# Kernel tuning notes

Measured on AMD Instinct MI355X. Metric: run time of the kernel, lower is better.

Reference implementation:

```python
import jax, jax.numpy as jnp
import numpy as np

SIGMA_D = 0.2
SIGMA_A = 15.0
FACTOR_A = 180.0 / (SIGMA_A * np.pi)
HIDDEN = 256


def sinusoidal_embedding(x, d_model):
    # GeoTransformer-style: interleaved sin/cos pairs along last dim.
    div_term = jnp.exp(jnp.arange(0, d_model, 2, dtype=x.dtype) * (-np.log(10000.0) / d_model))  # (d/2,)
    omegas = x[..., None] * div_term  # (..., d/2)
    emb = jnp.stack([jnp.sin(omegas), jnp.cos(omegas)], axis=-1)  # (..., d/2, 2)
    return emb.reshape(*x.shape, d_model)


def _indices(points, anchor_points):
    # pairwise sq dist: |p|^2 + |a|^2 - 2 p.a, clamped at 0
    sq = (jnp.sum(points ** 2, -1)[:, :, None]
          + jnp.sum(anchor_points ** 2, -1)[:, None, :]
          - 2.0 * jnp.einsum('bnd,bkd->bnk', points, anchor_points))
    dist_map = jnp.sqrt(jnp.maximum(sq, 0.0))  # (B,N,K)
    d_indices = dist_map / SIGMA_D
    ref_vectors = points[:, :, None, :] - anchor_points[:, None, :, :]  # (B,N,K,3)
    # gather with indices [1,2,...,K-1,0] == roll by -1 along K
    anc_vectors = jnp.roll(ref_vectors, shift=-1, axis=2)
    sin_values = jnp.linalg.norm(jnp.cross(ref_vectors, anc_vectors, axis=-1), axis=-1)
    cos_values = jnp.sum(ref_vectors * anc_vectors, axis=-1)
    angles = jnp.arctan2(sin_values, cos_values)
    a_indices = angles * FACTOR_A
    return d_indices, a_indices


def setup_inputs() -> dict:
    key = jax.random.key(0)
    ks = jax.random.split(key, 5)
    B, N, K, H = 1, 4096, 64, HIDDEN
    return {
        'points': jax.random.normal(ks[0], (B, N, 3), jnp.float32),
        'anchor_points': jax.random.normal(ks[1], (B, K, 3), jnp.float32),
        'cor_score': jax.random.uniform(ks[2], (K,), jnp.float32),
        'Wa': jax.random.normal(ks[3], (H, H), jnp.float32) * (1.0 / np.sqrt(H)),
        'ba': jnp.zeros((H,), jnp.float32),
        'Wd': jax.random.normal(ks[4], (H, H), jnp.float32) * (1.0 / np.sqrt(H)),
        'bd': jnp.zeros((H,), jnp.float32),
    }


def reference(points, anchor_points, cor_score, Wa, ba, Wd, bd):
    d_idx, a_idx = _indices(points, anchor_points)  # computed under no_grad in torch
    d_idx = jax.lax.stop_gradient(d_idx)
    a_idx = jax.lax.stop_gradient(a_idx)
    a_emb = sinusoidal_embedding(a_idx, HIDDEN)          # (B,N,K,H)
    a_emb = jnp.einsum('bnkh,oh->bnko', a_emb, Wa) + ba
    d_emb = sinusoidal_embedding(d_idx, HIDDEN)
    d_emb = jnp.einsum('bnkh,oh->bnko', d_emb, Wd) + bd
    # reduction_a == 'max'
    d_emb = jnp.max(d_emb, axis=2)
    a_emb = jnp.max(a_emb, axis=2)
    return d_emb + a_emb  # (B,N,H)
```

## Files before the change

kernel.cpp:

```cpp
#include <hip/hip_runtime.h>
#include <hip/hip_bf16.h>
#include <math.h>


typedef __attribute__((ext_vector_type(8))) short short8;
typedef __attribute__((ext_vector_type(16))) float f32x16;
typedef __attribute__((ext_vector_type(4))) unsigned int uint4v;

#define HH 256
#define KK 112
#define P_PTS 8
#define NPTS 4096

__device__ __forceinline__ unsigned short f2bf(float f) {
    union { float f; unsigned int u; } v; v.f = f;
    unsigned int r = v.u + 0x7fffu + ((v.u >> 16) & 1u);
    return (unsigned short)(r >> 16);
}

__device__ __forceinline__ unsigned int pack_sc(float s, float c) {
    union { __hip_bfloat162 h; unsigned int u; } v;
    v.h = __float22bfloat162_rn(make_float2(s, c));
    return v.u;
}

__global__ __launch_bounds__(256)
void prep_w_kernel(const float* __restrict__ Wa, const float* __restrict__ Wd,
                   unsigned short* __restrict__ wbf) {
    const int t = blockIdx.x;
    const int o = threadIdx.x;
    const float* W = (t == 0 ? Wd : Wa) + o * HH;
    unsigned short* dst = wbf + (t * HH + o) * KK;
    for (int e = 0; e < 104; ++e) dst[e] = f2bf(W[e]);
    float u1 = 0.f, u2 = 0.f, u3 = 0.f, u4 = 0.f, v = 0.f;
    for (int i = 52; i < 128; ++i) {
        const float d = exp2f(-(float)i * 0.10381025296523008f);
        const float d2 = d * d;
        const float ws = W[2 * i], wc = W[2 * i + 1];
        u1 += d * ws;
        u3 += -(d * d2) * (1.0f / 6.0f) * ws;
        u2 += -0.5f * d2 * wc;
        u4 += (d2 * d2) * (1.0f / 24.0f) * wc;
        v  += wc;
    }
    dst[104] = f2bf(u1);
    dst[105] = f2bf(u2);
    dst[106] = f2bf(u3);
    dst[107] = f2bf(u4);
    dst[108] = f2bf(v);
    dst[109] = 0; dst[110] = 0; dst[111] = 0;
}


__global__ __launch_bounds__(512, 4)
void cgse_main(const float* __restrict__ points,
               const float* __restrict__ anchors,
               const unsigned short* __restrict__ wbf,
               const float* __restrict__ ba,
               const float* __restrict__ bd,
               float* __restrict__ out) {
    __shared__ __align__(16) unsigned short E[2][64 * 128];
    __shared__ float dms[2][P_PTS][HH];
    __shared__ float ams[2][P_PTS][HH];
    __shared__ float xs[2][P_PTS][64];
    __shared__ float anch[192];

    const int tid = threadIdx.x;
    const int wave = tid >> 6, lane = tid & 63;
    const int l5 = lane & 31, half = lane >> 5;
    const int base = blockIdx.x * P_PTS;
    const int hh = wave >> 2;
    const int colb = (wave & 3) * 64;

    if (tid < 192) anch[tid] = anchors[tid];
    __syncthreads();
    {
        const int k2 = (lane + 1) & 63;
        const int pn = base + wave;
        const float px = points[pn * 3 + 0], py = points[pn * 3 + 1], pz = points[pn * 3 + 2];
        const float r1x = px - anch[lane * 3 + 0];
        const float r1y = py - anch[lane * 3 + 1];
        const float r1z = pz - anch[lane * 3 + 2];
        const float r2x = px - anch[k2 * 3 + 0];
        const float r2y = py - anch[k2 * 3 + 1];
        const float r2z = pz - anch[k2 * 3 + 2];
        xs[0][wave][lane] = sqrtf(r1x * r1x + r1y * r1y + r1z * r1z) * 5.0f;
        const float cx = r1y * r2z - r1z * r2y;
        const float cy = r1z * r2x - r1x * r2z;
        const float cz = r1x * r2y - r1y * r2x;
        const float sv = sqrtf(cx * cx + cy * cy + cz * cz);
        const float cv = r1x * r2x + r1y * r2y + r1z * r2z;
        xs[1][wave][lane] = atan2f(sv, cv) * 3.8197186342054885f;
    }

    const float bias_c = (tid < HH) ? (ba[tid] + bd[tid]) : 0.0f;

    const float cw = 0.15915494309189535f * __expf(-(float)wave * 0.2878231366242554f);

    const int wbase = (lane << 8) ^ (((lane & 7) ^ wave) << 4);
    const int arow = hh * 32 + l5;
    const int rbase = (arow << 8) ^ ((arow & 7) << 4) ^ (half << 4);

    auto fill_chunk = [&](char* eb, int c, float x, float xc) {
        uint4v w;
        if (wave == 5 && c == 1) {
            const float x2 = x * x;
            w[0] = pack_sc(x, x2);
            w[1] = pack_sc(x2 * x, x2 * x2);
            w[2] = pack_sc(1.0f, 0.0f);
            w[3] = 0u;
        } else {
            const float t0 = c ? xc * 0.1f : xc;
            const float t[4] = {t0, t0 * 0.9305720409297085f,
                                t0 * 0.8659643233600653f, t0 * 0.8058421877614819f};
            #pragma unroll
            for (int j = 0; j < 4; ++j)
                w[j] = pack_sc(__builtin_amdgcn_sinf(t[j]), __builtin_amdgcn_cosf(t[j]));
        }
        *(uint4v*)(eb + (wbase ^ (c << 7))) = w;
    };

    short8 bw[2][7];
    auto loadW = [&](int t) {
        #pragma unroll
        for (int ntp = 0; ntp < 2; ++ntp) {
            const unsigned short* wr =
                wbf + (t * HH + colb + ntp * 32 + l5) * KK + half * 8;
            #pragma unroll
            for (int ks = 0; ks < 7; ++ks)
                bw[ntp][ks] = *(const short8*)(wr + ks * 16);
        }
    };

    loadW(0);
    __syncthreads();
    {
        const float x = xs[0][0][lane], xc = x * cw;
        fill_chunk((char*)E[0], 0, x, xc);
        if (wave < 6) fill_chunk((char*)E[0], 1, x, xc);
    }

    #pragma unroll 1
    for (int ph = 0; ph < 17; ++ph) {
        __syncthreads();

        if (ph >= 9 && tid < HH) {
            const int q = ph - 9;
            out[(base + q) * HH + tid] =
                fmaxf(ams[0][q][tid], ams[1][q][tid]) +
                fmaxf(dms[0][q][tid], dms[1][q][tid]) + bias_c;
        }
        if (ph == 16) break;

        const int b = ph & 1;
        if (ph == 8) loadW(1);

        const bool dofill = (ph + 1) < 16;
        float xn = 0.f, xcn = 0.f;
        if (dofill) {
            const int pn = (ph + 1) & 7;
            xn = ((ph + 1) < 8 ? xs[0][pn][lane] : xs[1][pn][lane]);
            xcn = xn * cw;
        }

        const char* ebC = (const char*)E[b];
        char* ebN = (char*)E[b ^ 1];

        f32x16 acc[2];
        #pragma unroll
        for (int ntp = 0; ntp < 2; ++ntp)
            #pragma unroll
            for (int r = 0; r < 16; ++r) acc[ntp][r] = 0.f;

        #pragma unroll
        for (int ks = 0; ks < 7; ++ks) {
            if (dofill) {
                if (ks == 0) fill_chunk(ebN, 0, xn, xcn);
                if (ks == 3 && wave < 6) fill_chunk(ebN, 1, xn, xcn);
            }
            const short8 afr = *(const short8*)(ebC + (rbase ^ (ks << 5)));
            acc[0] = __builtin_amdgcn_mfma_f32_32x32x16_bf16(afr, bw[0][ks], acc[0], 0, 0, 0);
            acc[1] = __builtin_amdgcn_mfma_f32_32x32x16_bf16(afr, bw[1][ks], acc[1], 0, 0, 0);
        }

        const int q = ph & 7;
        float (*pm)[P_PTS][HH] = (ph < 8) ? dms : ams;
        #pragma unroll
        for (int ntp = 0; ntp < 2; ++ntp) {
            float t8[8];
            #pragma unroll
            for (int r = 0; r < 8; ++r)
                t8[r] = fmaxf(acc[ntp][2 * r], acc[ntp][2 * r + 1]);
            const float ta = fmaxf(fmaxf(t8[0], t8[1]), fmaxf(t8[2], t8[3]));
            const float tb = fmaxf(fmaxf(t8[4], t8[5]), fmaxf(t8[6], t8[7]));
            float m = fmaxf(ta, tb);
            m = fmaxf(m, __shfl_down(m, 32));
            if (lane < 32) pm[hh][q][colb + ntp * 32 + l5] = m;
        }
    }
}

extern "C" void kernel_launch(void* const* d_in, const int* in_sizes, int n_in,
                              void* d_out, int out_size, void* d_ws, size_t ws_size,
                              hipStream_t stream) {
    const float* points  = (const float*)d_in[0];
    const float* anchors = (const float*)d_in[1];
    const float* Wa = (const float*)d_in[3];
    const float* ba = (const float*)d_in[4];
    const float* Wd = (const float*)d_in[5];
    const float* bd = (const float*)d_in[6];

    unsigned short* wbf = (unsigned short*)d_ws;

    hipLaunchKernelGGL(prep_w_kernel, dim3(2), dim3(256), 0, stream, Wa, Wd, wbf);
    hipLaunchKernelGGL(cgse_main, dim3(NPTS / P_PTS), dim3(512), 0, stream,
                       points, anchors, wbf, ba, bd, (float*)d_out);
}
```

Baseline: 110.5 us.

## Halve points per block, raise occupancy, vectorize weight prep, prioritize MFMA

The main kernel now handles 4 points per block instead of 8, which doubles the grid, and its launch bounds now ask for 6 blocks per CU. The weight prep kernel spreads its work over 8 blocks of 64 threads, loads and converts weights in float4 vectors, and replaces the per-iteration exp2 with a running multiply. It also raises wave priority around the MFMA pair and regroups the max reduction into 3-input fmax ops. Each block still loads both weight sets, so fewer points per block means more weight reloads per point, and the tighter register budget may cause spills.

```diff
diff --git a/kernel.cpp b/kernel.cpp
--- a/kernel.cpp
+++ b/kernel.cpp
@@ -6,10 +6,12 @@
 typedef __attribute__((ext_vector_type(8))) short short8;
 typedef __attribute__((ext_vector_type(16))) float f32x16;
 typedef __attribute__((ext_vector_type(4))) unsigned int uint4v;
+typedef __attribute__((ext_vector_type(4))) float float4v;
+typedef __attribute__((ext_vector_type(4))) unsigned short ushort4v;
 
 #define HH 256
 #define KK 112
-#define P_PTS 8
+#define P_PTS 4
 #define NPTS 4096
 
 __device__ __forceinline__ unsigned short f2bf(float f) {
@@ -24,17 +26,24 @@
     return v.u;
 }
 
-__global__ __launch_bounds__(256)
+__global__ __launch_bounds__(64)
 void prep_w_kernel(const float* __restrict__ Wa, const float* __restrict__ Wd,
                    unsigned short* __restrict__ wbf) {
-    const int t = blockIdx.x;
-    const int o = threadIdx.x;
+    const int r = blockIdx.x * 64 + threadIdx.x;
+    const int t = r >> 8, o = r & 255;
     const float* W = (t == 0 ? Wd : Wa) + o * HH;
     unsigned short* dst = wbf + (t * HH + o) * KK;
-    for (int e = 0; e < 104; ++e) dst[e] = f2bf(W[e]);
+    #pragma unroll
+    for (int e4 = 0; e4 < 26; ++e4) {
+        const float4v w4 = *(const float4v*)(W + e4 * 4);
+        ushort4v s4;
+        #pragma unroll
+        for (int j = 0; j < 4; ++j) s4[j] = f2bf(w4[j]);
+        *(ushort4v*)(dst + e4 * 4) = s4;
+    }
     float u1 = 0.f, u2 = 0.f, u3 = 0.f, u4 = 0.f, v = 0.f;
+    float d = 0.023713737056616554f;
     for (int i = 52; i < 128; ++i) {
-        const float d = exp2f(-(float)i * 0.10381025296523008f);
         const float d2 = d * d;
         const float ws = W[2 * i], wc = W[2 * i + 1];
         u1 += d * ws;
@@ -42,6 +51,7 @@
         u2 += -0.5f * d2 * wc;
         u4 += (d2 * d2) * (1.0f / 24.0f) * wc;
         v  += wc;
+        d *= 0.9305720409297085f;
     }
     dst[104] = f2bf(u1);
     dst[105] = f2bf(u2);
@@ -52,7 +62,7 @@
 }
 
 
-__global__ __launch_bounds__(512, 4)
+__global__ __launch_bounds__(512, 6)
 void cgse_main(const float* __restrict__ points,
                const float* __restrict__ anchors,
                const unsigned short* __restrict__ wbf,
@@ -74,7 +84,7 @@
 
     if (tid < 192) anch[tid] = anchors[tid];
     __syncthreads();
-    {
+    if (wave < 4) {
         const int k2 = (lane + 1) & 63;
         const int pn = base + wave;
         const float px = points[pn * 3 + 0], py = points[pn * 3 + 1], pz = points[pn * 3 + 2];
@@ -141,25 +151,25 @@
     }
 
     #pragma unroll 1
-    for (int ph = 0; ph < 17; ++ph) {
+    for (int ph = 0; ph < 9; ++ph) {
         __syncthreads();
 
-        if (ph >= 9 && tid < HH) {
-            const int q = ph - 9;
+        if (ph >= 5 && tid < HH) {
+            const int q = ph - 5;
             out[(base + q) * HH + tid] =
                 fmaxf(ams[0][q][tid], ams[1][q][tid]) +
                 fmaxf(dms[0][q][tid], dms[1][q][tid]) + bias_c;
         }
-        if (ph == 16) break;
+        if (ph == 8) break;
 
         const int b = ph & 1;
-        if (ph == 8) loadW(1);
-
-        const bool dofill = (ph + 1) < 16;
+        if (ph == 4) loadW(1);
+
+        const bool dofill = (ph + 1) < 8;
         float xn = 0.f, xcn = 0.f;
         if (dofill) {
-            const int pn = (ph + 1) & 7;
-            xn = ((ph + 1) < 8 ? xs[0][pn][lane] : xs[1][pn][lane]);
+            const int pn = (ph + 1) & 3;
+            xn = ((ph + 1) < 4 ? xs[0][pn][lane] : xs[1][pn][lane]);
             xcn = xn * cw;
         }
 
@@ -179,21 +189,25 @@
                 if (ks == 3 && wave < 6) fill_chunk(ebN, 1, xn, xcn);
             }
             const short8 afr = *(const short8*)(ebC + (rbase ^ (ks << 5)));
+            __builtin_amdgcn_s_setprio(1);
             acc[0] = __builtin_amdgcn_mfma_f32_32x32x16_bf16(afr, bw[0][ks], acc[0], 0, 0, 0);
             acc[1] = __builtin_amdgcn_mfma_f32_32x32x16_bf16(afr, bw[1][ks], acc[1], 0, 0, 0);
-        }
-
-        const int q = ph & 7;
-        float (*pm)[P_PTS][HH] = (ph < 8) ? dms : ams;
+            __builtin_amdgcn_s_setprio(0);
+        }
+
+        const int q = ph & 3;
+        float (*pm)[P_PTS][HH] = (ph < 4) ? dms : ams;
         #pragma unroll
         for (int ntp = 0; ntp < 2; ++ntp) {
-            float t8[8];
-            #pragma unroll
-            for (int r = 0; r < 8; ++r)
-                t8[r] = fmaxf(acc[ntp][2 * r], acc[ntp][2 * r + 1]);
-            const float ta = fmaxf(fmaxf(t8[0], t8[1]), fmaxf(t8[2], t8[3]));
-            const float tb = fmaxf(fmaxf(t8[4], t8[5]), fmaxf(t8[6], t8[7]));
-            float m = fmaxf(ta, tb);
+            const f32x16& a = acc[ntp];
+            const float v0 = fmaxf(fmaxf(a[0], a[1]), a[2]);
+            const float v1 = fmaxf(fmaxf(a[3], a[4]), a[5]);
+            const float v2 = fmaxf(fmaxf(a[6], a[7]), a[8]);
+            const float v3 = fmaxf(fmaxf(a[9], a[10]), a[11]);
+            const float v4 = fmaxf(fmaxf(a[12], a[13]), a[14]);
+            const float w0 = fmaxf(fmaxf(v0, v1), v2);
+            const float w1 = fmaxf(fmaxf(v3, v4), a[15]);
+            float m = fmaxf(w0, w1);
             m = fmaxf(m, __shfl_down(m, 32));
             if (lane < 32) pm[hh][q][colb + ntp * 32 + l5] = m;
         }
@@ -212,7 +226,7 @@
 
     unsigned short* wbf = (unsigned short*)d_ws;
 
-    hipLaunchKernelGGL(prep_w_kernel, dim3(2), dim3(256), 0, stream, Wa, Wd, wbf);
+    hipLaunchKernelGGL(prep_w_kernel, dim3(8), dim3(64), 0, stream, Wa, Wd, wbf);
     hipLaunchKernelGGL(cgse_main, dim3(NPTS / P_PTS), dim3(512), 0, stream,
                        points, anchors, wbf, ba, bd, (float*)d_out);
 }
```

New measurement: 183.8 us. 66.4% more time.
